# Performance work log

Measured on AMD Instinct MI355X. Metric: run time of the kernel, lower is better.

The kernel has to match this reference:

```python
import jax, jax.numpy as jnp
import numpy as np

N_NODES = 100000
N_EDGES = 1600000
IN_CH = 128
HID_CH = 128


def setup_inputs() -> dict:
    key = jax.random.key(0)
    ks = jax.random.split(key, 12)
    s = 1.0 / np.sqrt(IN_CH)
    sh = 1.0 / np.sqrt(HID_CH)
    return {
        "x": jax.random.normal(ks[0], (N_NODES, IN_CH), dtype=jnp.float32),
        "edge_index": jax.random.randint(ks[1], (2, N_EDGES), 0, N_NODES, dtype=jnp.int32),
        # SAGEConv1: lin_l (applied to aggregated neighbors, has bias), lin_r (root)
        "W1_l": jax.random.uniform(ks[2], (IN_CH, HID_CH), jnp.float32, -s, s),
        "b1": jax.random.uniform(ks[3], (HID_CH,), jnp.float32, -s, s),
        "W1_r": jax.random.uniform(ks[4], (IN_CH, HID_CH), jnp.float32, -s, s),
        # SAGEConv2
        "W2_l": jax.random.uniform(ks[5], (HID_CH, HID_CH), jnp.float32, -sh, sh),
        "b2": jax.random.uniform(ks[6], (HID_CH,), jnp.float32, -sh, sh),
        "W2_r": jax.random.uniform(ks[7], (HID_CH, HID_CH), jnp.float32, -sh, sh),
        # decoder Linear(hidden, in)
        "Wd": jax.random.uniform(ks[8], (HID_CH, IN_CH), jnp.float32, -sh, sh),
        "bd": jax.random.uniform(ks[9], (IN_CH,), jnp.float32, -sh, sh),
        "alpha": jnp.float32(0.5),
    }


def _sage_conv(h, src, dst, n_nodes, W_l, b, W_r):
    # PyG SAGEConv (mean aggr): out = lin_l(mean_{j in N(i)} x_j) + lin_r(x_i)
    msg = h[src]  # [E, C] gather from source nodes
    agg = jax.ops.segment_sum(msg, dst, num_segments=n_nodes)  # [N, C]
    cnt = jax.ops.segment_sum(jnp.ones((src.shape[0],), h.dtype), dst,
                              num_segments=n_nodes)  # [N]
    mean = agg / jnp.maximum(cnt, 1.0)[:, None]
    return mean @ W_l + b + h @ W_r


def reference(x, edge_index, W1_l, b1, W1_r, W2_l, b2, W2_r, Wd, bd, alpha):
    n_nodes = x.shape[0]
    src, dst = edge_index[0], edge_index[1]
    h = jax.nn.relu(_sage_conv(x, src, dst, n_nodes, W1_l, b1, W1_r))
    # dropout p=0.2 is identity in eval mode
    h = jax.nn.relu(_sage_conv(h, src, dst, n_nodes, W2_l, b2, W2_r))
    x_updated = h @ Wd + bd
    return alpha * x_updated + (1.0 - alpha) * x
```

## Files before the change

### kernel.cpp

```cpp
#include <hip/hip_runtime.h>
#include <cstddef>
#include <cstdint>

#define CH 128
#define NBKT 196
#define ABLK 320
#define BKT_NODES 512

typedef __attribute__((ext_vector_type(8))) short short8;
typedef __attribute__((ext_vector_type(4))) float f32x4;

__device__ __forceinline__ unsigned short f2bf(float f) {
  unsigned u = __float_as_uint(f);
  u += 0x7FFF + ((u >> 16) & 1);
  return (unsigned short)(u >> 16);
}
__device__ __forceinline__ float bf_lo(unsigned int u) {
  return __uint_as_float(u << 16);
}
__device__ __forceinline__ float bf_hi(unsigned int u) {
  return __uint_as_float(u & 0xffff0000u);
}
__device__ __forceinline__ void gld16(const void* g, void* l) {
  __builtin_amdgcn_global_load_lds((const __attribute__((address_space(1))) unsigned int*)g,
                                   (__attribute__((address_space(3))) unsigned int*)l, 16, 0, 0);
}

__global__ void k_cvt(const float4* __restrict__ in, uint4* __restrict__ out, int n8) {
  int i = blockIdx.x * 256 + threadIdx.x;
  if (i < n8) {
    float4 a = in[i * 2], b = in[i * 2 + 1];
    uint4 o;
    o.x = (unsigned)f2bf(a.x) | ((unsigned)f2bf(a.y) << 16);
    o.y = (unsigned)f2bf(a.z) | ((unsigned)f2bf(a.w) << 16);
    o.z = (unsigned)f2bf(b.x) | ((unsigned)f2bf(b.y) << 16);
    o.w = (unsigned)f2bf(b.z) | ((unsigned)f2bf(b.w) << 16);
    out[i] = o;
  }
}

__global__ void k_wt(const float* __restrict__ w0, const float* __restrict__ w1,
                     const float* __restrict__ w2, const float* __restrict__ w3,
                     const float* __restrict__ w4, unsigned short* __restrict__ dst) {
  const float* srcs[5] = {w0, w1, w2, w3, w4};
  const float* w = srcs[blockIdx.x];
  unsigned short* d = dst + (size_t)blockIdx.x * CH * CH;
  for (int idx = threadIdx.x; idx < CH * CH; idx += 256) {
    int k = idx >> 7, nn = idx & 127;
    d[nn * CH + k] = f2bf(w[idx]);
  }
}

__global__ void k_bhist(const int* __restrict__ dst, int* __restrict__ cnt, int E, int chunk) {
  __shared__ int c[NBKT];
  for (int i = threadIdx.x; i < NBKT; i += 256) c[i] = 0;
  __syncthreads();
  int s = blockIdx.x * chunk;
  int e = min(s + chunk, E);
  for (int i = s + threadIdx.x; i < e; i += 256)
    atomicAdd(&c[dst[i] >> 9], 1);
  __syncthreads();
  for (int i = threadIdx.x; i < NBKT; i += 256)
    cnt[i * ABLK + blockIdx.x] = c[i];
}

__global__ void k_bin(const int* __restrict__ src, const int* __restrict__ dst,
                      const int* __restrict__ ofs, unsigned int* __restrict__ binned,
                      int E, int chunk) {
  __shared__ int cur[NBKT];
  for (int i = threadIdx.x; i < NBKT; i += 256) cur[i] = ofs[i * ABLK + blockIdx.x];
  __syncthreads();
  int s = blockIdx.x * chunk;
  int e = min(s + chunk, E);
  for (int i = s + threadIdx.x; i < e; i += 256) {
    int d = dst[i];
    int b = d >> 9;
    int pos = atomicAdd(&cur[b], 1);
    binned[pos] = (unsigned)src[i] | ((unsigned)(d & 511) << 17);
  }
}

__global__ __launch_bounds__(256)
void k_bucket(const unsigned int* __restrict__ binned, const int* __restrict__ ofs,
              int* __restrict__ rowptr, int* __restrict__ sorted, int N, int E, int nbkt) {
  __shared__ int c[BKT_NODES];
  __shared__ int tsum[256];
  __shared__ int cur[BKT_NODES];
  int b = blockIdx.x, t = threadIdx.x;
  int s = ofs[b * ABLK];
  int e = ofs[(b + 1) * ABLK];
  c[t] = 0; c[t + 256] = 0;
  __syncthreads();
  for (int i = s + t; i < e; i += 256)
    atomicAdd(&c[binned[i] >> 17], 1);
  __syncthreads();
  int v0 = c[2 * t], v1 = c[2 * t + 1];
  int tot = v0 + v1;
  tsum[t] = tot;
  __syncthreads();
  for (int o = 1; o < 256; o <<= 1) {
    int y = (t >= o) ? tsum[t - o] : 0;
    __syncthreads();
    tsum[t] += y;
    __syncthreads();
  }
  int excl = tsum[t] - tot;
  int base = b * BKT_NODES;
  int r0 = s + excl, r1 = s + excl + v0;
  if (base + 2 * t < N)     rowptr[base + 2 * t]     = r0;
  if (base + 2 * t + 1 < N) rowptr[base + 2 * t + 1] = r1;
  cur[2 * t] = r0; cur[2 * t + 1] = r1;
  __syncthreads();
  for (int i = s + t; i < e; i += 256) {
    unsigned w = binned[i];
    int pos = atomicAdd(&cur[w >> 17], 1);
    sorted[pos] = w & 0x1FFFF;
  }
  if (b == nbkt - 1 && t == 0) rowptr[N] = E;
}

__global__ void k_scan1(const int* __restrict__ deg, int* __restrict__ rowptr,
                        int* __restrict__ bsums, int n) {
  __shared__ int sh[256];
  int tid = threadIdx.x;
  int base = blockIdx.x * 1024 + tid * 4;
  int v0 = (base + 0 < n) ? deg[base + 0] : 0;
  int v1 = (base + 1 < n) ? deg[base + 1] : 0;
  int v2 = (base + 2 < n) ? deg[base + 2] : 0;
  int v3 = (base + 3 < n) ? deg[base + 3] : 0;
  int tot = v0 + v1 + v2 + v3;
  sh[tid] = tot;
  __syncthreads();
  for (int off = 1; off < 256; off <<= 1) {
    int y = (tid >= off) ? sh[tid - off] : 0;
    __syncthreads();
    sh[tid] += y;
    __syncthreads();
  }
  int excl = sh[tid] - tot;
  if (base + 0 < n) rowptr[base + 0] = excl;
  if (base + 1 < n) rowptr[base + 1] = excl + v0;
  if (base + 2 < n) rowptr[base + 2] = excl + v0 + v1;
  if (base + 3 < n) rowptr[base + 3] = excl + v0 + v1 + v2;
  if (tid == 255) bsums[blockIdx.x] = sh[255];
}

__global__ void k_scan2(int* __restrict__ bsums, int g) {
  __shared__ int sh[1024];
  int tid = threadIdx.x;
  int v = (tid < g) ? bsums[tid] : 0;
  sh[tid] = v;
  __syncthreads();
  for (int off = 1; off < 1024; off <<= 1) {
    int y = (tid >= off) ? sh[tid - off] : 0;
    __syncthreads();
    sh[tid] += y;
    __syncthreads();
  }
  if (tid < g) bsums[tid] = sh[tid] - v;
}

__global__ void k_scan3(int* __restrict__ arr, const int* __restrict__ bsums, int n, int total) {
  int i = blockIdx.x * 256 + threadIdx.x;
  if (i < n) arr[i] += bsums[i >> 10];
  if (i == 0) arr[n] = total;
}

__global__ __launch_bounds__(256)
void k_agg(const uint4* __restrict__ in4, uint4* __restrict__ out4,
           const int* __restrict__ rowptr, const int* __restrict__ sorted_src,
           int n, int nwaves) {
  int wid = (blockIdx.x * 256 + threadIdx.x) >> 6;
  int lane = threadIdx.x & 63;
  int quad = lane >> 4;
  int sl = lane & 15;

  for (int node = wid; node < n; node += nwaves) {
    int beg = rowptr[node], end = rowptr[node + 1];
    float a0 = 0.f, a1 = 0.f, a2 = 0.f, a3 = 0.f;
    float a4 = 0.f, a5 = 0.f, a6 = 0.f, a7 = 0.f;
    int e = beg;
    for (; e + 16 <= end; e += 16) {
      uint4 v[4];
#pragma unroll
      for (int j = 0; j < 4; j++)
        v[j] = in4[((unsigned)sorted_src[e + 4 * j + quad] << 4) + sl];
#pragma unroll
      for (int j = 0; j < 4; j++) {
        a0 += bf_lo(v[j].x); a1 += bf_hi(v[j].x);
        a2 += bf_lo(v[j].y); a3 += bf_hi(v[j].y);
        a4 += bf_lo(v[j].z); a5 += bf_hi(v[j].z);
        a6 += bf_lo(v[j].w); a7 += bf_hi(v[j].w);
      }
    }
    if (e < end) {
      uint4 v[4];
#pragma unroll
      for (int j = 0; j < 4; j++) {
        int k = e + 4 * j + quad;
        int idx = (k < end) ? k : beg;
        uint4 tv = in4[((unsigned)sorted_src[idx] << 4) + sl];
        if (k >= end) { tv.x = 0u; tv.y = 0u; tv.z = 0u; tv.w = 0u; }
        v[j] = tv;
      }
#pragma unroll
      for (int j = 0; j < 4; j++) {
        a0 += bf_lo(v[j].x); a1 += bf_hi(v[j].x);
        a2 += bf_lo(v[j].y); a3 += bf_hi(v[j].y);
        a4 += bf_lo(v[j].z); a5 += bf_hi(v[j].z);
        a6 += bf_lo(v[j].w); a7 += bf_hi(v[j].w);
      }
    }
    a0 += __shfl(a0, lane ^ 16); a1 += __shfl(a1, lane ^ 16);
    a2 += __shfl(a2, lane ^ 16); a3 += __shfl(a3, lane ^ 16);
    a4 += __shfl(a4, lane ^ 16); a5 += __shfl(a5, lane ^ 16);
    a6 += __shfl(a6, lane ^ 16); a7 += __shfl(a7, lane ^ 16);
    a0 += __shfl(a0, lane ^ 32); a1 += __shfl(a1, lane ^ 32);
    a2 += __shfl(a2, lane ^ 32); a3 += __shfl(a3, lane ^ 32);
    a4 += __shfl(a4, lane ^ 32); a5 += __shfl(a5, lane ^ 32);
    a6 += __shfl(a6, lane ^ 32); a7 += __shfl(a7, lane ^ 32);
    int d = end - beg;
    float inv = (d > 0) ? (1.f / (float)d) : 0.f;
    if (quad == 0) {
      uint4 o;
      o.x = (unsigned)f2bf(a0 * inv) | ((unsigned)f2bf(a1 * inv) << 16);
      o.y = (unsigned)f2bf(a2 * inv) | ((unsigned)f2bf(a3 * inv) << 16);
      o.z = (unsigned)f2bf(a4 * inv) | ((unsigned)f2bf(a5 * inv) << 16);
      o.w = (unsigned)f2bf(a6 * inv) | ((unsigned)f2bf(a7 * inv) << 16);
      out4[((unsigned)node << 4) + sl] = o;
    }
  }
}

__global__ __launch_bounds__(256, 2)
void k_sage(const unsigned short* __restrict__ Am, const unsigned short* __restrict__ Ax,
            const unsigned short* __restrict__ WTl, const unsigned short* __restrict__ WTr,
            const float* __restrict__ bias, unsigned short* __restrict__ out, int n) {
  __shared__ unsigned short sA[128 * 64];
  __shared__ unsigned short sB[128 * 64];
  int tid = threadIdx.x;
  int lane = tid & 63;
  int w = tid >> 6;
  int row0 = blockIdx.x * 128;
  int col_lo = lane & 15, quad = lane >> 4;
  int rx = col_lo & 7;

  f32x4 acc[2][8];
#pragma unroll
  for (int mt = 0; mt < 2; mt++)
#pragma unroll
    for (int nt = 0; nt < 8; nt++) acc[mt][nt] = (f32x4){0.f, 0.f, 0.f, 0.f};

  const unsigned short* As[4] = {Am, Am, Ax, Ax};
  const unsigned short* Bs[4] = {WTl, WTl, WTr, WTr};
  const int k0s[4] = {0, 64, 0, 64};

  for (int c = 0; c < 4; c++) {
    const unsigned short* Ap = As[c];
    const unsigned short* Bp = Bs[c];
    int k0 = k0s[c];
#pragma unroll
    for (int it = 0; it < 4; it++) {
      int flat = it * 256 + tid;
      int r = flat >> 3;
      int sl8 = flat & 7;
      int kof = (sl8 ^ (r & 7)) * 8;
      int gr = row0 + r;
      if (gr > n - 1) gr = n - 1;
      gld16(Ap + (size_t)gr * CH + k0 + kof, sA + flat * 8);
      gld16(Bp + (size_t)r * CH + k0 + kof, sB + flat * 8);
    }
    __syncthreads();

#pragma unroll
    for (int ks = 0; ks < 2; ks++) {
      int so = ((ks * 4 + quad) ^ rx) * 8;
      short8 a0 = *(const short8*)&sA[(w * 32 + col_lo) * 64 + so];
      short8 a1 = *(const short8*)&sA[(w * 32 + 16 + col_lo) * 64 + so];
      short8 b[8];
#pragma unroll
      for (int nt = 0; nt < 8; nt++)
        b[nt] = *(const short8*)&sB[(nt * 16 + col_lo) * 64 + so];
#pragma unroll
      for (int nt = 0; nt < 8; nt++) {
        acc[0][nt] = __builtin_amdgcn_mfma_f32_16x16x32_bf16(a0, b[nt], acc[0][nt], 0, 0, 0);
        acc[1][nt] = __builtin_amdgcn_mfma_f32_16x16x32_bf16(a1, b[nt], acc[1][nt], 0, 0, 0);
      }
    }
    __syncthreads();
  }

#pragma unroll
  for (int nt = 0; nt < 8; nt++) {
    float bb = bias[nt * 16 + col_lo];
#pragma unroll
    for (int mt = 0; mt < 2; mt++) {
#pragma unroll
      for (int r = 0; r < 4; r++) {
        int rr = row0 + w * 32 + mt * 16 + quad * 4 + r;
        if (rr < n) {
          float v = fmaxf(acc[mt][nt][r] + bb, 0.f);
          out[(size_t)rr * CH + nt * 16 + col_lo] = f2bf(v);
        }
      }
    }
  }
}

__global__ __launch_bounds__(256, 2)
void k_dec(const unsigned short* __restrict__ H, const unsigned short* __restrict__ WTd,
           const float* __restrict__ bd, const float* __restrict__ X,
           const float* __restrict__ alpha_p, float* __restrict__ out, int n) {
  __shared__ unsigned short sA[128 * 64];
  __shared__ unsigned short sB[128 * 64];
  int tid = threadIdx.x;
  int lane = tid & 63;
  int w = tid >> 6;
  int row0 = blockIdx.x * 128;
  int col_lo = lane & 15, quad = lane >> 4;
  int rx = col_lo & 7;

  f32x4 acc[2][8];
#pragma unroll
  for (int mt = 0; mt < 2; mt++)
#pragma unroll
    for (int nt = 0; nt < 8; nt++) acc[mt][nt] = (f32x4){0.f, 0.f, 0.f, 0.f};

  for (int c = 0; c < 2; c++) {
    int k0 = c * 64;
#pragma unroll
    for (int it = 0; it < 4; it++) {
      int flat = it * 256 + tid;
      int r = flat >> 3;
      int sl8 = flat & 7;
      int kof = (sl8 ^ (r & 7)) * 8;
      int gr = row0 + r;
      if (gr > n - 1) gr = n - 1;
      gld16(H + (size_t)gr * CH + k0 + kof, sA + flat * 8);
      gld16(WTd + (size_t)r * CH + k0 + kof, sB + flat * 8);
    }
    __syncthreads();

#pragma unroll
    for (int ks = 0; ks < 2; ks++) {
      int so = ((ks * 4 + quad) ^ rx) * 8;
      short8 a0 = *(const short8*)&sA[(w * 32 + col_lo) * 64 + so];
      short8 a1 = *(const short8*)&sA[(w * 32 + 16 + col_lo) * 64 + so];
      short8 b[8];
#pragma unroll
      for (int nt = 0; nt < 8; nt++)
        b[nt] = *(const short8*)&sB[(nt * 16 + col_lo) * 64 + so];
#pragma unroll
      for (int nt = 0; nt < 8; nt++) {
        acc[0][nt] = __builtin_amdgcn_mfma_f32_16x16x32_bf16(a0, b[nt], acc[0][nt], 0, 0, 0);
        acc[1][nt] = __builtin_amdgcn_mfma_f32_16x16x32_bf16(a1, b[nt], acc[1][nt], 0, 0, 0);
      }
    }
    __syncthreads();
  }

  float al = alpha_p[0];
  float be = 1.f - al;
#pragma unroll
  for (int nt = 0; nt < 8; nt++) {
    float bb = bd[nt * 16 + col_lo];
#pragma unroll
    for (int mt = 0; mt < 2; mt++) {
#pragma unroll
      for (int r = 0; r < 4; r++) {
        int rr = row0 + w * 32 + mt * 16 + quad * 4 + r;
        if (rr < n) {
          int cc = nt * 16 + col_lo;
          float xv = X[(size_t)rr * CH + cc];
          out[(size_t)rr * CH + cc] = al * (acc[mt][nt][r] + bb) + be * xv;
        }
      }
    }
  }
}


extern "C" void kernel_launch(void* const* d_in, const int* in_sizes, int n_in,
                              void* d_out, int out_size, void* d_ws, size_t ws_size,
                              hipStream_t stream) {
  const float* x   = (const float*)d_in[0];
  const int*   ei  = (const int*)d_in[1];
  const float* W1l = (const float*)d_in[2];
  const float* b1  = (const float*)d_in[3];
  const float* W1r = (const float*)d_in[4];
  const float* W2l = (const float*)d_in[5];
  const float* b2  = (const float*)d_in[6];
  const float* W2r = (const float*)d_in[7];
  const float* Wd  = (const float*)d_in[8];
  const float* bd  = (const float*)d_in[9];
  const float* alp = (const float*)d_in[10];

  int N = in_sizes[0] / CH;
  int E = in_sizes[1] / 2;
  const int* src = ei;
  const int* dst = ei + E;

  char* ws = (char*)d_ws;
  size_t off = 0;
  auto alloc = [&](size_t bytes) -> char* {
    off = (off + 511) & ~size_t(511);
    char* p = ws + off;
    off += bytes;
    return p;
  };
  int*   rowptr = (int*)alloc((size_t)(N + 1) * 4);
  int*   ofs    = (int*)alloc((size_t)(NBKT * ABLK + 1) * 4);
  int*   bsums  = (int*)alloc(4096);
  int*   sorted = (int*)alloc((size_t)E * 4);
  unsigned short* xb = (unsigned short*)alloc((size_t)N * CH * 2);
  unsigned short* h  = (unsigned short*)alloc((size_t)N * CH * 2);
  unsigned short* WT = (unsigned short*)alloc((size_t)5 * CH * CH * 2);
  unsigned short* mean = (unsigned short*)d_out;
  unsigned int* binned = (unsigned int*)((char*)d_out + (size_t)N * CH * 2);

  int chunk = (E + ABLK - 1) / ABLK;
  int nA = NBKT * ABLK;
  int GA = (nA + 1023) / 1024;

  k_cvt<<<(N * CH / 8 + 255) / 256, 256, 0, stream>>>((const float4*)x, (uint4*)xb, N * CH / 8);
  k_wt<<<5, 256, 0, stream>>>(W1l, W1r, W2l, W2r, Wd, WT);

  k_bhist<<<ABLK, 256, 0, stream>>>(dst, ofs, E, chunk);
  k_scan1<<<GA, 256, 0, stream>>>(ofs, ofs, bsums, nA);
  k_scan2<<<1, 1024, 0, stream>>>(bsums, GA);
  k_scan3<<<(nA + 255) / 256, 256, 0, stream>>>(ofs, bsums, nA, E);
  k_bin<<<ABLK, 256, 0, stream>>>(src, dst, ofs, binned, E, chunk);
  k_bucket<<<NBKT, 256, 0, stream>>>(binned, ofs, rowptr, sorted, N, E, NBKT);

  int gAggBlocks = 2048;
  int nWaves = gAggBlocks * 4;
  int gGemm = (N + 127) / 128;
  unsigned short* WT1l = WT + 0 * CH * CH;
  unsigned short* WT1r = WT + 1 * CH * CH;
  unsigned short* WT2l = WT + 2 * CH * CH;
  unsigned short* WT2r = WT + 3 * CH * CH;
  unsigned short* WTd  = WT + 4 * CH * CH;

  k_agg<<<gAggBlocks, 256, 0, stream>>>((const uint4*)xb, (uint4*)mean, rowptr, sorted, N, nWaves);
  k_sage<<<gGemm, 256, 0, stream>>>(mean, xb, WT1l, WT1r, b1, h, N);
  k_agg<<<gAggBlocks, 256, 0, stream>>>((const uint4*)h, (uint4*)mean, rowptr, sorted, N, nWaves);
  k_sage<<<gGemm, 256, 0, stream>>>(mean, h, WT2l, WT2r, b2, h, N);
  k_dec<<<gGemm, 256, 0, stream>>>(h, WTd, bd, x, alp, (float*)d_out, N);
}
```

Baseline: 411.7 us.

## Double-buffer A tiles in LDS and read weights directly from global

The GEMM kernels k_sage and k_dec now double-buffer the activation tile in LDS, prefetching the next K chunk while MFMAs run on the current one. Weight B fragments are read straight from global memory (expected to hit in cache) instead of being staged through LDS. The launch-bounds minimum-occupancy hint is dropped. This trades LDS staging for global/L2 reads of the weights, and may raise register pressure. The loop's remaining __syncthreads between iterations is not shown, so whether the buffer swap is synchronised correctly is uncertain.

```diff
diff --git a/kernel.cpp b/kernel.cpp
--- a/kernel.cpp
+++ b/kernel.cpp
@@ -232,12 +232,11 @@
   }
 }
 
-__global__ __launch_bounds__(256, 2)
+__global__ __launch_bounds__(256)
 void k_sage(const unsigned short* __restrict__ Am, const unsigned short* __restrict__ Ax,
             const unsigned short* __restrict__ WTl, const unsigned short* __restrict__ WTr,
             const float* __restrict__ bias, unsigned short* __restrict__ out, int n) {
-  __shared__ unsigned short sA[128 * 64];
-  __shared__ unsigned short sB[128 * 64];
+  __shared__ unsigned short sA[2][128 * 64];
   int tid = threadIdx.x;
   int lane = tid & 63;
   int w = tid >> 6;
@@ -255,32 +254,45 @@
   const unsigned short* Bs[4] = {WTl, WTl, WTr, WTr};
   const int k0s[4] = {0, 64, 0, 64};
 
+#pragma unroll
+  for (int it = 0; it < 4; it++) {
+    int flat = it * 256 + tid;
+    int r = flat >> 3;
+    int sl8 = flat & 7;
+    int kof = (sl8 ^ (r & 7)) * 8;
+    int gr = row0 + r;
+    if (gr > n - 1) gr = n - 1;
+    gld16(As[0] + (size_t)gr * CH + k0s[0] + kof, sA[0] + flat * 8);
+  }
+  __syncthreads();
+
   for (int c = 0; c < 4; c++) {
-    const unsigned short* Ap = As[c];
+    int cur = c & 1;
+    if (c < 3) {
+      const unsigned short* Ap = As[c + 1];
+      int k0n = k0s[c + 1];
+#pragma unroll
+      for (int it = 0; it < 4; it++) {
+        int flat = it * 256 + tid;
+        int r = flat >> 3;
+        int sl8 = flat & 7;
+        int kof = (sl8 ^ (r & 7)) * 8;
+        int gr = row0 + r;
+        if (gr > n - 1) gr = n - 1;
+        gld16(Ap + (size_t)gr * CH + k0n + kof, sA[cur ^ 1] + flat * 8);
+      }
+    }
     const unsigned short* Bp = Bs[c];
     int k0 = k0s[c];
 #pragma unroll
-    for (int it = 0; it < 4; it++) {
-      int flat = it * 256 + tid;
-      int r = flat >> 3;
-      int sl8 = flat & 7;
-      int kof = (sl8 ^ (r & 7)) * 8;
-      int gr = row0 + r;
-      if (gr > n - 1) gr = n - 1;
-      gld16(Ap + (size_t)gr * CH + k0 + kof, sA + flat * 8);
-      gld16(Bp + (size_t)r * CH + k0 + kof, sB + flat * 8);
-    }
-    __syncthreads();
-
-#pragma unroll
     for (int ks = 0; ks < 2; ks++) {
       int so = ((ks * 4 + quad) ^ rx) * 8;
-      short8 a0 = *(const short8*)&sA[(w * 32 + col_lo) * 64 + so];
-      short8 a1 = *(const short8*)&sA[(w * 32 + 16 + col_lo) * 64 + so];
+      short8 a0 = *(const short8*)&sA[cur][(w * 32 + col_lo) * 64 + so];
+      short8 a1 = *(const short8*)&sA[cur][(w * 32 + 16 + col_lo) * 64 + so];
       short8 b[8];
 #pragma unroll
       for (int nt = 0; nt < 8; nt++)
-        b[nt] = *(const short8*)&sB[(nt * 16 + col_lo) * 64 + so];
+        b[nt] = *(const short8*)&Bp[(size_t)(nt * 16 + col_lo) * CH + k0 + ks * 32 + quad * 8];
 #pragma unroll
       for (int nt = 0; nt < 8; nt++) {
         acc[0][nt] = __builtin_amdgcn_mfma_f32_16x16x32_bf16(a0, b[nt], acc[0][nt], 0, 0, 0);
@@ -307,12 +319,11 @@
   }
 }
 
-__global__ __launch_bounds__(256, 2)
+__global__ __launch_bounds__(256)
 void k_dec(const unsigned short* __restrict__ H, const unsigned short* __restrict__ WTd,
            const float* __restrict__ bd, const float* __restrict__ X,
            const float* __restrict__ alpha_p, float* __restrict__ out, int n) {
-  __shared__ unsigned short sA[128 * 64];
-  __shared__ unsigned short sB[128 * 64];
+  __shared__ unsigned short sA[2][128 * 64];
   int tid = threadIdx.x;
   int lane = tid & 63;
   int w = tid >> 6;
@@ -326,30 +337,42 @@
 #pragma unroll
     for (int nt = 0; nt < 8; nt++) acc[mt][nt] = (f32x4){0.f, 0.f, 0.f, 0.f};
 
+#pragma unroll
+  for (int it = 0; it < 4; it++) {
+    int flat = it * 256 + tid;
+    int r = flat >> 3;
+    int sl8 = flat & 7;
+    int kof = (sl8 ^ (r & 7)) * 8;
+    int gr = row0 + r;
+    if (gr > n - 1) gr = n - 1;
+    gld16(H + (size_t)gr * CH + 0 + kof, sA[0] + flat * 8);
+  }
+  __syncthreads();
+
   for (int c = 0; c < 2; c++) {
+    int cur = c & 1;
+    if (c < 1) {
+#pragma unroll
+      for (int it = 0; it < 4; it++) {
+        int flat = it * 256 + tid;
+        int r = flat >> 3;
+        int sl8 = flat & 7;
+        int kof = (sl8 ^ (r & 7)) * 8;
+        int gr = row0 + r;
+        if (gr > n - 1) gr = n - 1;
+        gld16(H + (size_t)gr * CH + 64 + kof, sA[cur ^ 1] + flat * 8);
+      }
+    }
     int k0 = c * 64;
-#pragma unroll
-    for (int it = 0; it < 4; it++) {
-      int flat = it * 256 + tid;
-      int r = flat >> 3;
-      int sl8 = flat & 7;
-      int kof = (sl8 ^ (r & 7)) * 8;
-      int gr = row0 + r;
-      if (gr > n - 1) gr = n - 1;
-      gld16(H + (size_t)gr * CH + k0 + kof, sA + flat * 8);
-      gld16(WTd + (size_t)r * CH + k0 + kof, sB + flat * 8);
-    }
-    __syncthreads();
-
 #pragma unroll
     for (int ks = 0; ks < 2; ks++) {
       int so = ((ks * 4 + quad) ^ rx) * 8;
-      short8 a0 = *(const short8*)&sA[(w * 32 + col_lo) * 64 + so];
-      short8 a1 = *(const short8*)&sA[(w * 32 + 16 + col_lo) * 64 + so];
+      short8 a0 = *(const short8*)&sA[cur][(w * 32 + col_lo) * 64 + so];
+      short8 a1 = *(const short8*)&sA[cur][(w * 32 + 16 + col_lo) * 64 + so];
       short8 b[8];
 #pragma unroll
       for (int nt = 0; nt < 8; nt++)
-        b[nt] = *(const short8*)&sB[(nt * 16 + col_lo) * 64 + so];
+        b[nt] = *(const short8*)&WTd[(size_t)(nt * 16 + col_lo) * CH + k0 + ks * 32 + quad * 8];
 #pragma unroll
       for (int nt = 0; nt < 8; nt++) {
         acc[0][nt] = __builtin_amdgcn_mfma_f32_16x16x32_bf16(a0, b[nt], acc[0][nt], 0, 0, 0);
```

Result: slower. 486.1 us (+18.1%).

## Fuse preprocessing kernels and replace bucket offset scan with atomic fixed-capacity bins

Applied to the files above, without the earlier changes.

Merges the bf16 conversion, weight transpose and counter reset into one launch. The histogram and binning passes become one kernel that reserves space per bucket with global atomics into fixed-capacity slots. This removes the three-kernel prefix scan, cutting launch count and the per-block offset table. The cost is non-deterministic edge order within a bucket and a fixed capacity of 10240 per bucket, which overflows if a bucket receives more edges than that (about 8192 expected here).

```diff
diff --git a/kernel.cpp b/kernel.cpp
--- a/kernel.cpp
+++ b/kernel.cpp
@@ -6,6 +6,7 @@
 #define NBKT 196
 #define ABLK 320
 #define BKT_NODES 512
+#define BKTCAP 10240
 
 typedef __attribute__((ext_vector_type(8))) short short8;
 typedef __attribute__((ext_vector_type(4))) float f32x4;
@@ -26,33 +27,41 @@
                                    (__attribute__((address_space(3))) unsigned int*)l, 16, 0, 0);
 }
 
-__global__ void k_cvt(const float4* __restrict__ in, uint4* __restrict__ out, int n8) {
-  int i = blockIdx.x * 256 + threadIdx.x;
-  if (i < n8) {
-    float4 a = in[i * 2], b = in[i * 2 + 1];
-    uint4 o;
-    o.x = (unsigned)f2bf(a.x) | ((unsigned)f2bf(a.y) << 16);
-    o.y = (unsigned)f2bf(a.z) | ((unsigned)f2bf(a.w) << 16);
-    o.z = (unsigned)f2bf(b.x) | ((unsigned)f2bf(b.y) << 16);
-    o.w = (unsigned)f2bf(b.z) | ((unsigned)f2bf(b.w) << 16);
-    out[i] = o;
-  }
-}
-
-__global__ void k_wt(const float* __restrict__ w0, const float* __restrict__ w1,
-                     const float* __restrict__ w2, const float* __restrict__ w3,
-                     const float* __restrict__ w4, unsigned short* __restrict__ dst) {
-  const float* srcs[5] = {w0, w1, w2, w3, w4};
-  const float* w = srcs[blockIdx.x];
-  unsigned short* d = dst + (size_t)blockIdx.x * CH * CH;
-  for (int idx = threadIdx.x; idx < CH * CH; idx += 256) {
-    int k = idx >> 7, nn = idx & 127;
-    d[nn * CH + k] = f2bf(w[idx]);
-  }
-}
-
-__global__ void k_bhist(const int* __restrict__ dst, int* __restrict__ cnt, int E, int chunk) {
+__global__ void k_pre(const float4* __restrict__ in, uint4* __restrict__ out, int n8,
+                      const float* __restrict__ w0, const float* __restrict__ w1,
+                      const float* __restrict__ w2, const float* __restrict__ w3,
+                      const float* __restrict__ w4, unsigned short* __restrict__ wdst,
+                      int* __restrict__ cnt) {
+  int b = blockIdx.x;
+  if (b < 5) {
+    const float* srcs[5] = {w0, w1, w2, w3, w4};
+    const float* w = srcs[b];
+    unsigned short* d = wdst + (size_t)b * CH * CH;
+    for (int idx = threadIdx.x; idx < CH * CH; idx += 256) {
+      int k = idx >> 7, nn = idx & 127;
+      d[nn * CH + k] = f2bf(w[idx]);
+    }
+  } else if (b == 5) {
+    if (threadIdx.x < NBKT) cnt[threadIdx.x] = 0;
+  } else {
+    int i = (b - 6) * 256 + threadIdx.x;
+    if (i < n8) {
+      float4 a = in[i * 2], c = in[i * 2 + 1];
+      uint4 o;
+      o.x = (unsigned)f2bf(a.x) | ((unsigned)f2bf(a.y) << 16);
+      o.y = (unsigned)f2bf(a.z) | ((unsigned)f2bf(a.w) << 16);
+      o.z = (unsigned)f2bf(c.x) | ((unsigned)f2bf(c.y) << 16);
+      o.w = (unsigned)f2bf(c.z) | ((unsigned)f2bf(c.w) << 16);
+      out[i] = o;
+    }
+  }
+}
+
+__global__ void k_binfused(const int* __restrict__ src, const int* __restrict__ dst,
+                           int* __restrict__ cnt, unsigned int* __restrict__ binned,
+                           int E, int chunk) {
   __shared__ int c[NBKT];
+  __shared__ int curq[NBKT];
   for (int i = threadIdx.x; i < NBKT; i += 256) c[i] = 0;
   __syncthreads();
   int s = blockIdx.x * chunk;
@@ -61,38 +70,41 @@
     atomicAdd(&c[dst[i] >> 9], 1);
   __syncthreads();
   for (int i = threadIdx.x; i < NBKT; i += 256)
-    cnt[i * ABLK + blockIdx.x] = c[i];
-}
-
-__global__ void k_bin(const int* __restrict__ src, const int* __restrict__ dst,
-                      const int* __restrict__ ofs, unsigned int* __restrict__ binned,
-                      int E, int chunk) {
-  __shared__ int cur[NBKT];
-  for (int i = threadIdx.x; i < NBKT; i += 256) cur[i] = ofs[i * ABLK + blockIdx.x];
-  __syncthreads();
-  int s = blockIdx.x * chunk;
-  int e = min(s + chunk, E);
+    curq[i] = atomicAdd(&cnt[i], c[i]);
+  __syncthreads();
   for (int i = s + threadIdx.x; i < e; i += 256) {
     int d = dst[i];
     int b = d >> 9;
-    int pos = atomicAdd(&cur[b], 1);
-    binned[pos] = (unsigned)src[i] | ((unsigned)(d & 511) << 17);
+    int pos = atomicAdd(&curq[b], 1);
+    binned[(size_t)b * BKTCAP + pos] = (unsigned)src[i] | ((unsigned)(d & 511) << 17);
   }
 }
 
 __global__ __launch_bounds__(256)
-void k_bucket(const unsigned int* __restrict__ binned, const int* __restrict__ ofs,
+void k_bucket(const unsigned int* __restrict__ binned, const int* __restrict__ cnt,
               int* __restrict__ rowptr, int* __restrict__ sorted, int N, int E, int nbkt) {
   __shared__ int c[BKT_NODES];
   __shared__ int tsum[256];
   __shared__ int cur[BKT_NODES];
+  __shared__ int bscan[256];
   int b = blockIdx.x, t = threadIdx.x;
-  int s = ofs[b * ABLK];
-  int e = ofs[(b + 1) * ABLK];
+  int cv = (t < nbkt) ? cnt[t] : 0;
+  bscan[t] = cv;
+  __syncthreads();
+  for (int o = 1; o < 256; o <<= 1) {
+    int y = (t >= o) ? bscan[t - o] : 0;
+    __syncthreads();
+    bscan[t] += y;
+    __syncthreads();
+  }
+  int cntb = cnt[b];
+  int gbase = bscan[b] - cntb;
+  size_t sread = (size_t)b * BKTCAP;
+
   c[t] = 0; c[t + 256] = 0;
   __syncthreads();
-  for (int i = s + t; i < e; i += 256)
-    atomicAdd(&c[binned[i] >> 17], 1);
+  for (int i = t; i < cntb; i += 256)
+    atomicAdd(&c[binned[sread + i] >> 17], 1);
   __syncthreads();
   int v0 = c[2 * t], v1 = c[2 * t + 1];
   int tot = v0 + v1;
@@ -106,64 +118,17 @@
   }
   int excl = tsum[t] - tot;
   int base = b * BKT_NODES;
-  int r0 = s + excl, r1 = s + excl + v0;
+  int r0 = gbase + excl, r1 = gbase + excl + v0;
   if (base + 2 * t < N)     rowptr[base + 2 * t]     = r0;
   if (base + 2 * t + 1 < N) rowptr[base + 2 * t + 1] = r1;
   cur[2 * t] = r0; cur[2 * t + 1] = r1;
   __syncthreads();
-  for (int i = s + t; i < e; i += 256) {
-    unsigned w = binned[i];
+  for (int i = t; i < cntb; i += 256) {
+    unsigned w = binned[sread + i];
     int pos = atomicAdd(&cur[w >> 17], 1);
     sorted[pos] = w & 0x1FFFF;
   }
   if (b == nbkt - 1 && t == 0) rowptr[N] = E;
-}
-
-__global__ void k_scan1(const int* __restrict__ deg, int* __restrict__ rowptr,
-                        int* __restrict__ bsums, int n) {
-  __shared__ int sh[256];
-  int tid = threadIdx.x;
-  int base = blockIdx.x * 1024 + tid * 4;
-  int v0 = (base + 0 < n) ? deg[base + 0] : 0;
-  int v1 = (base + 1 < n) ? deg[base + 1] : 0;
-  int v2 = (base + 2 < n) ? deg[base + 2] : 0;
-  int v3 = (base + 3 < n) ? deg[base + 3] : 0;
-  int tot = v0 + v1 + v2 + v3;
-  sh[tid] = tot;
-  __syncthreads();
-  for (int off = 1; off < 256; off <<= 1) {
-    int y = (tid >= off) ? sh[tid - off] : 0;
-    __syncthreads();
-    sh[tid] += y;
-    __syncthreads();
-  }
-  int excl = sh[tid] - tot;
-  if (base + 0 < n) rowptr[base + 0] = excl;
-  if (base + 1 < n) rowptr[base + 1] = excl + v0;
-  if (base + 2 < n) rowptr[base + 2] = excl + v0 + v1;
-  if (base + 3 < n) rowptr[base + 3] = excl + v0 + v1 + v2;
-  if (tid == 255) bsums[blockIdx.x] = sh[255];
-}
-
-__global__ void k_scan2(int* __restrict__ bsums, int g) {
-  __shared__ int sh[1024];
-  int tid = threadIdx.x;
-  int v = (tid < g) ? bsums[tid] : 0;
-  sh[tid] = v;
-  __syncthreads();
-  for (int off = 1; off < 1024; off <<= 1) {
-    int y = (tid >= off) ? sh[tid - off] : 0;
-    __syncthreads();
-    sh[tid] += y;
-    __syncthreads();
-  }
-  if (tid < g) bsums[tid] = sh[tid] - v;
-}
-
-__global__ void k_scan3(int* __restrict__ arr, const int* __restrict__ bsums, int n, int total) {
-  int i = blockIdx.x * 256 + threadIdx.x;
-  if (i < n) arr[i] += bsums[i >> 10];
-  if (i == 0) arr[n] = total;
 }
 
 __global__ __launch_bounds__(256)
@@ -409,8 +374,7 @@
     return p;
   };
   int*   rowptr = (int*)alloc((size_t)(N + 1) * 4);
-  int*   ofs    = (int*)alloc((size_t)(NBKT * ABLK + 1) * 4);
-  int*   bsums  = (int*)alloc(4096);
+  int*   cnt    = (int*)alloc((size_t)NBKT * 4);
   int*   sorted = (int*)alloc((size_t)E * 4);
   unsigned short* xb = (unsigned short*)alloc((size_t)N * CH * 2);
   unsigned short* h  = (unsigned short*)alloc((size_t)N * CH * 2);
@@ -419,18 +383,13 @@
   unsigned int* binned = (unsigned int*)((char*)d_out + (size_t)N * CH * 2);
 
   int chunk = (E + ABLK - 1) / ABLK;
-  int nA = NBKT * ABLK;
-  int GA = (nA + 1023) / 1024;
-
-  k_cvt<<<(N * CH / 8 + 255) / 256, 256, 0, stream>>>((const float4*)x, (uint4*)xb, N * CH / 8);
-  k_wt<<<5, 256, 0, stream>>>(W1l, W1r, W2l, W2r, Wd, WT);
-
-  k_bhist<<<ABLK, 256, 0, stream>>>(dst, ofs, E, chunk);
-  k_scan1<<<GA, 256, 0, stream>>>(ofs, ofs, bsums, nA);
-  k_scan2<<<1, 1024, 0, stream>>>(bsums, GA);
-  k_scan3<<<(nA + 255) / 256, 256, 0, stream>>>(ofs, bsums, nA, E);
-  k_bin<<<ABLK, 256, 0, stream>>>(src, dst, ofs, binned, E, chunk);
-  k_bucket<<<NBKT, 256, 0, stream>>>(binned, ofs, rowptr, sorted, N, E, NBKT);
+  int n8 = N * CH / 8;
+  int gCvt = (n8 + 255) / 256;
+
+  k_pre<<<6 + gCvt, 256, 0, stream>>>((const float4*)x, (uint4*)xb, n8,
+                                      W1l, W1r, W2l, W2r, Wd, WT, cnt);
+  k_binfused<<<ABLK, 256, 0, stream>>>(src, dst, cnt, binned, E, chunk);
+  k_bucket<<<NBKT, 256, 0, stream>>>(binned, cnt, rowptr, sorted, N, E, NBKT);
 
   int gAggBlocks = 2048;
   int nWaves = gAggBlocks * 4;
```

Result: faster. 397.0 us (-3.6%).
